# Performance work log

Measured on AMD Instinct MI355X. Metric: run time of the kernel, lower is better.

The kernel has to match this reference:

```python
import jax, jax.numpy as jnp
import numpy as np

E = 1024      # embed_dim
H = 16        # num_heads
HD = E // H   # head_dim = 64
R = 8         # dora rank
T, B = 2048, 2


def setup_inputs() -> dict:
    key = jax.random.key(0)
    ks = jax.random.split(key, 16)
    query = jax.random.normal(ks[0], (T, B, E), dtype=jnp.float32)
    kk = jax.random.normal(ks[1], (T, B, E), dtype=jnp.float32)
    vv = jax.random.normal(ks[2], (T, B, E), dtype=jnp.float32)

    def make_dora(k1, k2, k3, k4):
        w = jax.random.normal(k1, (E, E), dtype=jnp.float32) * (E ** -0.5)
        m = jnp.linalg.norm(w)            # magnitude scalar (Frobenius norm)
        V = w / m                          # frozen direction, ||V||_F = 1
        A = jax.random.normal(k2, (R, E), dtype=jnp.float32) * (E ** -0.5)
        Bm = jax.random.normal(k3, (E, R), dtype=jnp.float32) * 0.01
        b = jax.random.normal(k4, (E,), dtype=jnp.float32) * 0.01
        return m, V, A, Bm, b

    mag_q, dir_q, A_q, B_q, bias_q = make_dora(ks[3], ks[4], ks[5], ks[6])
    mag_v, dir_v, A_v, B_v, bias_v = make_dora(ks[7], ks[8], ks[9], ks[10])
    k_w = jax.random.normal(ks[11], (E, E), dtype=jnp.float32) * (E ** -0.5)
    k_b = jax.random.normal(ks[12], (E,), dtype=jnp.float32) * 0.01
    out_w = jax.random.normal(ks[13], (E, E), dtype=jnp.float32) * (E ** -0.5)
    out_b = jax.random.normal(ks[14], (E,), dtype=jnp.float32) * 0.01
    return dict(query=query, key=kk, value=vv,
                mag_q=mag_q, dir_q=dir_q, A_q=A_q, B_q=B_q, bias_q=bias_q,
                mag_v=mag_v, dir_v=dir_v, A_v=A_v, B_v=B_v, bias_v=bias_v,
                k_w=k_w, k_b=k_b, out_w=out_w, out_b=out_b)


def _dora_linear(x, m, V, A, Bm, b):
    # W_eff = m * (V + B@A) / (||V + B@A||_F + 1e-8); out = x @ W_eff.T + b
    Vu = V + Bm @ A                      # [E, E]
    W = (m / (jnp.linalg.norm(Vu) + 1e-8)) * Vu
    return x @ W.T + b


def reference(query, key, value, mag_q, dir_q, A_q, B_q, bias_q,
              mag_v, dir_v, A_v, B_v, bias_v, k_w, k_b, out_w, out_b):
    # NOTE: source module ignores `key`/`value` and derives k, v from `query`.
    Tq, Bq, _ = query.shape
    q = _dora_linear(query, mag_q, dir_q, A_q, B_q, bias_q)   # [T, B, E]
    k = query @ k_w.T + k_b                                    # frozen K proj
    v = _dora_linear(query, mag_v, dir_v, A_v, B_v, bias_v)
    # (T, B, E) -> (B*H, T, HD), matching torch reshape/transpose
    q = q.reshape(Tq, Bq * H, HD).transpose(1, 0, 2)
    k = k.reshape(Tq, Bq * H, HD).transpose(1, 0, 2)
    v = v.reshape(Tq, Bq * H, HD).transpose(1, 0, 2)
    scale = HD ** -0.5
    attn = jnp.einsum('nqd,nkd->nqk', q, k) * scale            # [B*H, T, T]
    attn = jax.nn.softmax(attn, axis=-1)                       # dropout p=0
    out = jnp.einsum('nqk,nkd->nqd', attn, v)                  # [B*H, T, HD]
    out = out.transpose(1, 0, 2).reshape(Tq, Bq, E)
    out = out @ out_w.T + out_b
    return out
```

## Files before the change

kernel.cpp:

```cpp
#include <hip/hip_runtime.h>
#include <hip/hip_bf16.h>

#define E_DIM 1024
#define T_DIM 2048
#define B_DIM 2
#define H_DIM 16
#define HD_DIM 64
#define R_DIM 8
#define M_ROWS (T_DIM * B_DIM)
#define LOG2E 1.4426950408889634f

typedef __attribute__((ext_vector_type(8))) short bf16x8;
typedef __attribute__((ext_vector_type(4))) short bf16x4;
typedef __attribute__((ext_vector_type(4))) float f32x4;
typedef __attribute__((ext_vector_type(2))) unsigned uint2v;

#if __has_builtin(__builtin_amdgcn_exp2f)
#define EXP2F(x) __builtin_amdgcn_exp2f(x)
#else
#define EXP2F(x) exp2f(x)
#endif

__device__ __forceinline__ unsigned short f2bf(float f) {
  unsigned int u = __builtin_bit_cast(unsigned int, f);
  u += 0x7FFFu + ((u >> 16) & 1u);
  return (unsigned short)(u >> 16);
}

__device__ __forceinline__ unsigned cvt_pk_bf16(float lo, float hi) {
  unsigned r;
  asm("v_cvt_pk_bf16_f32 %0, %1, %2" : "=v"(r) : "v"(lo), "v"(hi));
  return r;
}

__device__ __forceinline__ f32x4 mfma16(bf16x4 a, bf16x4 b, f32x4 c) {
#if __has_builtin(__builtin_amdgcn_mfma_f32_16x16x16bf16_1k)
  return __builtin_amdgcn_mfma_f32_16x16x16bf16_1k(a, b, c, 0, 0, 0);
#elif __has_builtin(__builtin_amdgcn_mfma_f32_16x16x16_bf16)
  return __builtin_amdgcn_mfma_f32_16x16x16_bf16(a, b, c, 0, 0, 0);
#else
  asm("v_mfma_f32_16x16x16_bf16 %0, %1, %2, %0" : "+v"(c) : "v"(a), "v"(b));
  return c;
#endif
}

__device__ __forceinline__ void glds16(const unsigned short* g, unsigned short* l) {
  __builtin_amdgcn_global_load_lds(
      (__attribute__((address_space(1))) void*)(g),
      (__attribute__((address_space(3))) void*)(l), 16, 0, 0);
}

__global__ __launch_bounds__(256) void prep(
    const float* __restrict__ query, const float* __restrict__ k_w,
    const float* __restrict__ out_w,
    const float* __restrict__ dir_q, const float* __restrict__ A_q, const float* __restrict__ B_q,
    const float* __restrict__ dir_v, const float* __restrict__ A_v, const float* __restrict__ B_v,
    unsigned short* __restrict__ qA_bf, unsigned short* __restrict__ kw_bf,
    unsigned short* __restrict__ ow_bf,
    unsigned short* __restrict__ Wq, unsigned short* __restrict__ Wv,
    float* __restrict__ partials) {
  const int bid = blockIdx.x;
  if (bid < 6144) {
    int u = bid * 256 + threadIdx.x;
    const float* src;
    unsigned short* dst;
    if (u < 1048576) { src = query; dst = qA_bf; }
    else if (u < 1310720) { src = k_w; dst = kw_bf; u -= 1048576; }
    else { src = out_w; dst = ow_bf; u -= 1310720; }
    float4 f = reinterpret_cast<const float4*>(src)[u];
    ushort4 o;
    o.x = f2bf(f.x); o.y = f2bf(f.y); o.z = f2bf(f.z); o.w = f2bf(f.w);
    reinterpret_cast<ushort4*>(dst)[u] = o;
    return;
  }
  const int bid2 = bid - 6144;
  const int mat = bid2 >> 8, bx = bid2 & 255;
  const float* __restrict__ dir = mat ? dir_v : dir_q;
  const float* __restrict__ Am  = mat ? A_v   : A_q;
  const float* __restrict__ Bm  = mat ? B_v   : B_q;
  unsigned short* __restrict__ W = mat ? Wv : Wq;

  float sum = 0.0f;
  for (int idx = bx * 256 + threadIdx.x; idx < E_DIM * E_DIM; idx += 256 * 256) {
    int i = idx >> 10;
    int j = idx & (E_DIM - 1);
    float v = dir[idx];
#pragma unroll
    for (int r = 0; r < R_DIM; ++r)
      v += Bm[i * R_DIM + r] * Am[r * E_DIM + j];
    W[idx] = f2bf(v);
    sum += v * v;
  }
#pragma unroll
  for (int off = 32; off > 0; off >>= 1) sum += __shfl_down(sum, off);
  __shared__ float red[4];
  if ((threadIdx.x & 63) == 0) red[threadIdx.x >> 6] = sum;
  __syncthreads();
  if (threadIdx.x == 0)
    partials[mat * 256 + bx] = (red[0] + red[1]) + (red[2] + red[3]);
}

__global__ __launch_bounds__(256) void dora_pass2(
    const float* __restrict__ partials, const float* __restrict__ mag_q,
    const float* __restrict__ mag_v, float* __restrict__ scales) {
  __shared__ float red[4];
  for (int mat = 0; mat < 2; ++mat) {
    float s = partials[mat * 256 + threadIdx.x];
#pragma unroll
    for (int off = 32; off > 0; off >>= 1) s += __shfl_down(s, off);
    if ((threadIdx.x & 63) == 0) red[threadIdx.x >> 6] = s;
    __syncthreads();
    if (threadIdx.x == 0) {
      float tot = (red[0] + red[1]) + (red[2] + red[3]);
      float m = mat ? mag_v[0] : mag_q[0];
      scales[mat] = m / (sqrtf(tot) + 1e-8f);
    }
    __syncthreads();
  }
}

template <int OUT_MODE>
__device__ __forceinline__ void gemm_bt_core(
    const unsigned short* __restrict__ A, const unsigned short* __restrict__ W,
    const float* __restrict__ bias, float scale, float bscale,
    void* __restrict__ Cptr, int bm, int bn) {
  __shared__ unsigned short As[128 * 32];
  __shared__ unsigned short Bs[128 * 32];
  const int tid = threadIdx.x;
  const int w = tid >> 6, lane = tid & 63;
  const int lr = lane & 15, lg = lane >> 4;
  const int wm = w >> 1, wn = w & 1;

  f32x4 acc[4][4];
#pragma unroll
  for (int i = 0; i < 4; ++i)
#pragma unroll
    for (int j = 0; j < 4; ++j) acc[i][j] = (f32x4){0.f, 0.f, 0.f, 0.f};

  const int c0u = tid, c1u = 256 + tid;
  const int r0 = c0u >> 2, o0 = (c0u & 3) * 8;
  const int r1 = c1u >> 2, o1 = (c1u & 3) * 8;

  for (int k0 = 0; k0 < E_DIM; k0 += 32) {
    glds16(A + (size_t)(bm + r0) * E_DIM + k0 + o0, As + c0u * 8);
    glds16(W + (size_t)(bn + r0) * E_DIM + k0 + o0, Bs + c0u * 8);
    glds16(A + (size_t)(bm + r1) * E_DIM + k0 + o1, As + c1u * 8);
    glds16(W + (size_t)(bn + r1) * E_DIM + k0 + o1, Bs + c1u * 8);
    __syncthreads();

    bf16x8 af[4], bf[4];
#pragma unroll
    for (int i = 0; i < 4; ++i)
      af[i] = *reinterpret_cast<const bf16x8*>(As + (wm * 64 + i * 16 + lr) * 32 + lg * 8);
#pragma unroll
    for (int j = 0; j < 4; ++j)
      bf[j] = *reinterpret_cast<const bf16x8*>(Bs + (wn * 64 + j * 16 + lr) * 32 + lg * 8);
#pragma unroll
    for (int i = 0; i < 4; ++i)
#pragma unroll
      for (int j = 0; j < 4; ++j)
        acc[i][j] = __builtin_amdgcn_mfma_f32_16x16x32_bf16(af[i], bf[j], acc[i][j], 0, 0, 0);
    __syncthreads();
  }

  if (OUT_MODE == 2) {
#pragma unroll
    for (int i = 0; i < 4; ++i) {
      int rowbase = bm + wm * 64 + i * 16 + lg * 4;
      float4 bb = *reinterpret_cast<const float4*>(&bias[rowbase]);
      float bbv[4] = {bb.x, bb.y, bb.z, bb.w};
#pragma unroll
      for (int j = 0; j < 4; ++j) {
        int xrow = bn + wn * 64 + j * 16 + lr;
        int t = xrow >> 1, bsel = xrow & 1;
#pragma unroll
        for (int rr = 0; rr < 4; ++rr) {
          int wrow = rowbase + rr;
          float v = scale * acc[i][j][rr] + bbv[rr];
          int nn = (bsel << 4) | (wrow >> 6);
          int d = wrow & 63;
          reinterpret_cast<unsigned short*>(Cptr)[((size_t)nn * HD_DIM + d) * T_DIM + t] = f2bf(v);
        }
      }
    }
  } else {
#pragma unroll
    for (int i = 0; i < 4; ++i) {
      int row = bm + wm * 64 + i * 16 + lg * 4;
#pragma unroll
      for (int j = 0; j < 4; ++j) {
        int col = bn + wn * 64 + j * 16 + lr;
        float bv = bias[col] * bscale;
#pragma unroll
        for (int r = 0; r < 4; ++r) {
          float v = scale * acc[i][j][r] + bv;
          if (OUT_MODE == 1)
            reinterpret_cast<unsigned short*>(Cptr)[(size_t)(row + r) * E_DIM + col] = f2bf(v);
          else
            reinterpret_cast<float*>(Cptr)[(size_t)(row + r) * E_DIM + col] = v;
        }
      }
    }
  }
}

__global__ __launch_bounds__(256) void gemm_qkv(
    const unsigned short* __restrict__ Abf,
    const unsigned short* __restrict__ Wq, const unsigned short* __restrict__ Wk,
    const unsigned short* __restrict__ Wv,
    const float* __restrict__ bias_q, const float* __restrict__ k_b,
    const float* __restrict__ bias_v, const float* __restrict__ scales,
    unsigned short* __restrict__ qbuf, unsigned short* __restrict__ kbuf,
    unsigned short* __restrict__ vT) {
  const int bid = blockIdx.x;
  const int swz = (bid & 7) * 96 + (bid >> 3);
  if (swz < 512) {
    const int mat = swz >> 8;
    const int idx = swz & 255;
    const int bm = (idx >> 3) * 128, bn = (idx & 7) * 128;
    if (mat == 0) {
      const float sm = 0.125f * LOG2E;
      gemm_bt_core<1>(Abf, Wq, bias_q, scales[0] * sm, sm, qbuf, bm, bn);
    } else {
      gemm_bt_core<1>(Abf, Wk, k_b, 1.0f, 1.0f, kbuf, bm, bn);
    }
  } else {
    const int idx = swz - 512;
    gemm_bt_core<2>(Wv, Abf, bias_v, scales[1], 1.0f, vT,
                    (idx >> 5) * 128, (idx & 31) * 128);
  }
}

__global__ __launch_bounds__(256) void gemm_out(
    const unsigned short* __restrict__ Abf, const unsigned short* __restrict__ Wo,
    const float* __restrict__ bias, float* __restrict__ out) {
  const int bid = blockIdx.x;
  const int swz = (bid & 7) * 32 + (bid >> 3);
  gemm_bt_core<0>(Abf, Wo, bias, 1.0f, 1.0f, out, (swz >> 3) * 128, (swz & 7) * 128);
}

#define LDP 72

__global__ __launch_bounds__(512, 2) void attn_mfma(
    const unsigned short* __restrict__ qb, const unsigned short* __restrict__ kb,
    const unsigned short* __restrict__ vT, unsigned short* __restrict__ ob) {
  __shared__ unsigned short Ks[64 * LDP];
  __shared__ unsigned short Vt[64 * LDP];
  const int n = blockIdx.y, b = n >> 4, col0 = (n & 15) * HD_DIM;
  const int tid = threadIdx.x, w = tid >> 6, lane = tid & 63;
  const int lr = lane & 15, lg = lane >> 4;
  const int q0 = blockIdx.x * 256 + w * 32;

  bf16x8 qf[2][2];
#pragma unroll
  for (int rf = 0; rf < 2; ++rf)
#pragma unroll
    for (int ks = 0; ks < 2; ++ks)
      qf[rf][ks] = *reinterpret_cast<const bf16x8*>(
          qb + ((size_t)(q0 + rf * 16 + lr) * B_DIM + b) * E_DIM + col0 + ks * 32 + lg * 8);

  f32x4 accO[2][4];
#pragma unroll
  for (int rf = 0; rf < 2; ++rf)
#pragma unroll
    for (int df = 0; df < 4; ++df) accO[rf][df] = (f32x4){0.f, 0.f, 0.f, 0.f};
  float mrun0 = -1e30f, mrun1 = -1e30f, lrun0 = 0.f, lrun1 = 0.f;

  const int sr = tid >> 3, sc = (tid & 7) * 8;
  float4 rk, rv;
  rk = *reinterpret_cast<const float4*>(kb + ((size_t)sr * B_DIM + b) * E_DIM + col0 + sc);
  rv = *reinterpret_cast<const float4*>(vT + ((size_t)n * HD_DIM + sr) * T_DIM + sc);

  for (int kt = 0; kt < T_DIM; kt += 64) {
    __syncthreads();
    *reinterpret_cast<float4*>(Ks + sr * LDP + sc) = rk;
    *reinterpret_cast<float4*>(Vt + sr * LDP + sc) = rv;
    __syncthreads();
    if (kt + 64 < T_DIM) {
      int kt2 = kt + 64;
      rk = *reinterpret_cast<const float4*>(kb + ((size_t)(kt2 + sr) * B_DIM + b) * E_DIM + col0 + sc);
      rv = *reinterpret_cast<const float4*>(vT + ((size_t)n * HD_DIM + sr) * T_DIM + kt2 + sc);
    }

    f32x4 s[4][2];
#pragma unroll
    for (int kf = 0; kf < 4; ++kf)
#pragma unroll
      for (int rf = 0; rf < 2; ++rf) s[kf][rf] = (f32x4){0.f, 0.f, 0.f, 0.f};
    __builtin_amdgcn_s_setprio(1);
#pragma unroll
    for (int ks = 0; ks < 2; ++ks)
#pragma unroll
      for (int kf = 0; kf < 4; ++kf) {
        bf16x8 kfr = *reinterpret_cast<const bf16x8*>(Ks + (kf * 16 + lr) * LDP + ks * 32 + lg * 8);
#pragma unroll
        for (int rf = 0; rf < 2; ++rf)
          s[kf][rf] = __builtin_amdgcn_mfma_f32_16x16x32_bf16(kfr, qf[rf][ks], s[kf][rf], 0, 0, 0);
      }
    __builtin_amdgcn_s_setprio(0);

    float pm0, pm1;
    {
      float a0 = fmaxf(fmaxf(s[0][0][0], s[0][0][1]), fmaxf(s[0][0][2], s[0][0][3]));
      float a1 = fmaxf(fmaxf(s[1][0][0], s[1][0][1]), fmaxf(s[1][0][2], s[1][0][3]));
      float a2 = fmaxf(fmaxf(s[2][0][0], s[2][0][1]), fmaxf(s[2][0][2], s[2][0][3]));
      float a3 = fmaxf(fmaxf(s[3][0][0], s[3][0][1]), fmaxf(s[3][0][2], s[3][0][3]));
      pm0 = fmaxf(fmaxf(a0, a1), fmaxf(a2, a3));
      float b0 = fmaxf(fmaxf(s[0][1][0], s[0][1][1]), fmaxf(s[0][1][2], s[0][1][3]));
      float b1 = fmaxf(fmaxf(s[1][1][0], s[1][1][1]), fmaxf(s[1][1][2], s[1][1][3]));
      float b2 = fmaxf(fmaxf(s[2][1][0], s[2][1][1]), fmaxf(s[2][1][2], s[2][1][3]));
      float b3 = fmaxf(fmaxf(s[3][1][0], s[3][1][1]), fmaxf(s[3][1][2], s[3][1][3]));
      pm1 = fmaxf(fmaxf(b0, b1), fmaxf(b2, b3));
    }
    pm0 = fmaxf(pm0, __shfl_xor(pm0, 16)); pm0 = fmaxf(pm0, __shfl_xor(pm0, 32));
    pm1 = fmaxf(pm1, __shfl_xor(pm1, 16)); pm1 = fmaxf(pm1, __shfl_xor(pm1, 32));

    const int resc = __any((pm0 > mrun0 + 8.0f) || (pm1 > mrun1 + 8.0f));
    float mn0 = mrun0, mn1 = mrun1;
    if (resc) { mn0 = fmaxf(mn0, pm0); mn1 = fmaxf(mn1, pm1); }

#pragma unroll
    for (int kf = 0; kf < 4; ++kf)
#pragma unroll
      for (int r = 0; r < 4; ++r) {
        s[kf][0][r] = EXP2F(s[kf][0][r] - mn0);
        s[kf][1][r] = EXP2F(s[kf][1][r] - mn1);
      }

    bf16x4 pa4[2][4];
#pragma unroll
    for (int rf = 0; rf < 2; ++rf)
#pragma unroll
      for (int kf = 0; kf < 4; ++kf) {
        uint2v u = (uint2v){cvt_pk_bf16(s[kf][rf][0], s[kf][rf][1]),
                            cvt_pk_bf16(s[kf][rf][2], s[kf][rf][3])};
        pa4[rf][kf] = __builtin_bit_cast(bf16x4, u);
      }

    f32x4 u0 = (s[0][0] + s[1][0]) + (s[2][0] + s[3][0]);
    f32x4 u1 = (s[0][1] + s[1][1]) + (s[2][1] + s[3][1]);
    float ps0 = (u0[0] + u0[1]) + (u0[2] + u0[3]);
    float ps1 = (u1[0] + u1[1]) + (u1[2] + u1[3]);
    ps0 += __shfl_xor(ps0, 16); ps0 += __shfl_xor(ps0, 32);
    ps1 += __shfl_xor(ps1, 16); ps1 += __shfl_xor(ps1, 32);

    if (resc) {
      float al0 = EXP2F(mrun0 - mn0), al1 = EXP2F(mrun1 - mn1);
      mrun0 = mn0; mrun1 = mn1;
      lrun0 = lrun0 * al0 + ps0; lrun1 = lrun1 * al1 + ps1;
#pragma unroll
      for (int r = 0; r < 4; ++r) {
        float a0 = __shfl(al0, (lg << 2) | r);
        float a1 = __shfl(al1, (lg << 2) | r);
#pragma unroll
        for (int df = 0; df < 4; ++df) { accO[0][df][r] *= a0; accO[1][df][r] *= a1; }
      }
    } else {
      lrun0 += ps0; lrun1 += ps1;
    }

    __builtin_amdgcn_s_setprio(1);
#pragma unroll
    for (int kf = 0; kf < 4; ++kf) {
#pragma unroll
      for (int df = 0; df < 4; ++df) {
        bf16x4 vf4 = *reinterpret_cast<const bf16x4*>(
            Vt + (df * 16 + lr) * LDP + kf * 16 + lg * 4);
        accO[0][df] = mfma16(pa4[0][kf], vf4, accO[0][df]);
        accO[1][df] = mfma16(pa4[1][kf], vf4, accO[1][df]);
      }
    }
    __builtin_amdgcn_s_setprio(0);
  }

#pragma unroll
  for (int rf = 0; rf < 2; ++rf)
#pragma unroll
    for (int r = 0; r < 4; ++r) {
      float lv = __shfl(rf ? lrun1 : lrun0, (lg << 2) | r);
      float inv = 1.0f / lv;
      int row = q0 + rf * 16 + lg * 4 + r;
      size_t base = ((size_t)row * B_DIM + b) * E_DIM + col0;
#pragma unroll
      for (int df = 0; df < 4; ++df)
        ob[base + df * 16 + lr] = f2bf(accO[rf][df][r] * inv);
    }
}

extern "C" void kernel_launch(void* const* d_in, const int* in_sizes, int n_in,
                              void* d_out, int out_size, void* d_ws, size_t ws_size,
                              hipStream_t stream) {
  const float* query  = (const float*)d_in[0];
  const float* mag_q  = (const float*)d_in[3];
  const float* dir_q  = (const float*)d_in[4];
  const float* A_q    = (const float*)d_in[5];
  const float* B_q    = (const float*)d_in[6];
  const float* bias_q = (const float*)d_in[7];
  const float* mag_v  = (const float*)d_in[8];
  const float* dir_v  = (const float*)d_in[9];
  const float* A_v    = (const float*)d_in[10];
  const float* B_v    = (const float*)d_in[11];
  const float* bias_v = (const float*)d_in[12];
  const float* k_w    = (const float*)d_in[13];
  const float* k_b    = (const float*)d_in[14];
  const float* out_w  = (const float*)d_in[15];
  const float* out_b  = (const float*)d_in[16];
  float* out = (float*)d_out;

  char* ws = (char*)d_ws;
  float* partials = (float*)ws;
  float* scales   = (float*)(ws + 2048);
  unsigned short* qA_bf = (unsigned short*)(ws + 4096);
  unsigned short* wq_bf = qA_bf + (size_t)M_ROWS * E_DIM;
  unsigned short* wv_bf = wq_bf + (size_t)E_DIM * E_DIM;
  unsigned short* kw_bf = wv_bf + (size_t)E_DIM * E_DIM;
  unsigned short* ow_bf = kw_bf + (size_t)E_DIM * E_DIM;
  unsigned short* qbuf  = ow_bf + (size_t)E_DIM * E_DIM;
  unsigned short* kbuf  = qbuf + (size_t)M_ROWS * E_DIM;
  unsigned short* vTbuf = kbuf + (size_t)M_ROWS * E_DIM;
  unsigned short* abuf  = vTbuf + (size_t)M_ROWS * E_DIM;

  prep<<<6656, 256, 0, stream>>>(query, k_w, out_w,
                                 dir_q, A_q, B_q, dir_v, A_v, B_v,
                                 qA_bf, kw_bf, ow_bf, wq_bf, wv_bf, partials);
  dora_pass2<<<1, 256, 0, stream>>>(partials, mag_q, mag_v, scales);

  gemm_qkv<<<768, 256, 0, stream>>>(qA_bf, wq_bf, kw_bf, wv_bf,
                                    bias_q, k_b, bias_v, scales,
                                    qbuf, kbuf, vTbuf);
  attn_mfma<<<dim3(T_DIM / 256, B_DIM * H_DIM), 512, 0, stream>>>(
      qbuf, kbuf, vTbuf, abuf);
  gemm_out<<<256, 256, 0, stream>>>(abuf, ow_bf, out_b, out);
}
```

Before: 161.1 us.

## Fold DoRA norm reduction into QKV GEMM and double attention KV tile

```diff
diff --git a/kernel.cpp b/kernel.cpp
--- a/kernel.cpp
+++ b/kernel.cpp
@@ -100,25 +100,6 @@
     partials[mat * 256 + bx] = (red[0] + red[1]) + (red[2] + red[3]);
 }
 
-__global__ __launch_bounds__(256) void dora_pass2(
-    const float* __restrict__ partials, const float* __restrict__ mag_q,
-    const float* __restrict__ mag_v, float* __restrict__ scales) {
-  __shared__ float red[4];
-  for (int mat = 0; mat < 2; ++mat) {
-    float s = partials[mat * 256 + threadIdx.x];
-#pragma unroll
-    for (int off = 32; off > 0; off >>= 1) s += __shfl_down(s, off);
-    if ((threadIdx.x & 63) == 0) red[threadIdx.x >> 6] = s;
-    __syncthreads();
-    if (threadIdx.x == 0) {
-      float tot = (red[0] + red[1]) + (red[2] + red[3]);
-      float m = mat ? mag_v[0] : mag_q[0];
-      scales[mat] = m / (sqrtf(tot) + 1e-8f);
-    }
-    __syncthreads();
-  }
-}
-
 template <int OUT_MODE>
 __device__ __forceinline__ void gemm_bt_core(
     const unsigned short* __restrict__ A, const unsigned short* __restrict__ W,
@@ -209,24 +190,47 @@
     const unsigned short* __restrict__ Wq, const unsigned short* __restrict__ Wk,
     const unsigned short* __restrict__ Wv,
     const float* __restrict__ bias_q, const float* __restrict__ k_b,
-    const float* __restrict__ bias_v, const float* __restrict__ scales,
+    const float* __restrict__ bias_v,
+    const float* __restrict__ partials, const float* __restrict__ mag_q,
+    const float* __restrict__ mag_v,
     unsigned short* __restrict__ qbuf, unsigned short* __restrict__ kbuf,
     unsigned short* __restrict__ vT) {
   const int bid = blockIdx.x;
   const int swz = (bid & 7) * 96 + (bid >> 3);
-  if (swz < 512) {
-    const int mat = swz >> 8;
-    const int idx = swz & 255;
-    const int bm = (idx >> 3) * 128, bn = (idx & 7) * 128;
+  const int mat = (swz < 256) ? 0 : (swz < 512) ? 1 : 2;
+
+  float scale = 1.0f, bscale = 1.0f;
+  if (mat != 1) {
+    const int sel = (mat == 0) ? 0 : 1;
+    float s = partials[sel * 256 + threadIdx.x];
+#pragma unroll
+    for (int off = 32; off > 0; off >>= 1) s += __shfl_down(s, off);
+    __shared__ float red[4];
+    if ((threadIdx.x & 63) == 0) red[threadIdx.x >> 6] = s;
+    __syncthreads();
+    float tot = (red[0] + red[1]) + (red[2] + red[3]);
+    float m = (mat == 0) ? mag_q[0] : mag_v[0];
+    float sc = m / (sqrtf(tot) + 1e-8f);
     if (mat == 0) {
       const float sm = 0.125f * LOG2E;
-      gemm_bt_core<1>(Abf, Wq, bias_q, scales[0] * sm, sm, qbuf, bm, bn);
+      scale = sc * sm; bscale = sm;
     } else {
-      gemm_bt_core<1>(Abf, Wk, k_b, 1.0f, 1.0f, kbuf, bm, bn);
-    }
+      scale = sc;
+    }
+    __syncthreads();
+  }
+
+  if (mat == 0) {
+    const int idx = swz;
+    gemm_bt_core<1>(Abf, Wq, bias_q, scale, bscale, qbuf,
+                    (idx >> 3) * 128, (idx & 7) * 128);
+  } else if (mat == 1) {
+    const int idx = swz - 256;
+    gemm_bt_core<1>(Abf, Wk, k_b, 1.0f, 1.0f, kbuf,
+                    (idx >> 3) * 128, (idx & 7) * 128);
   } else {
     const int idx = swz - 512;
-    gemm_bt_core<2>(Wv, Abf, bias_v, scales[1], 1.0f, vT,
+    gemm_bt_core<2>(Wv, Abf, bias_v, scale, 1.0f, vT,
                     (idx >> 5) * 128, (idx & 31) * 128);
   }
 }
@@ -239,13 +243,14 @@
   gemm_bt_core<0>(Abf, Wo, bias, 1.0f, 1.0f, out, (swz >> 3) * 128, (swz & 7) * 128);
 }
 
-#define LDP 72
+#define LDPK 72
+#define LDPV 136
 
 __global__ __launch_bounds__(512, 2) void attn_mfma(
     const unsigned short* __restrict__ qb, const unsigned short* __restrict__ kb,
     const unsigned short* __restrict__ vT, unsigned short* __restrict__ ob) {
-  __shared__ unsigned short Ks[64 * LDP];
-  __shared__ unsigned short Vt[64 * LDP];
+  __shared__ unsigned short Ks2[128 * LDPK];
+  __shared__ unsigned short Vt2[64 * LDPV];
   const int n = blockIdx.y, b = n >> 4, col0 = (n & 15) * HD_DIM;
   const int tid = threadIdx.x, w = tid >> 6, lane = tid & 63;
   const int lr = lane & 15, lg = lane >> 4;
@@ -266,111 +271,126 @@
     for (int df = 0; df < 4; ++df) accO[rf][df] = (f32x4){0.f, 0.f, 0.f, 0.f};
   float mrun0 = -1e30f, mrun1 = -1e30f, lrun0 = 0.f, lrun1 = 0.f;
 
-  const int sr = tid >> 3, sc = (tid & 7) * 8;
-  float4 rk, rv;
-  rk = *reinterpret_cast<const float4*>(kb + ((size_t)sr * B_DIM + b) * E_DIM + col0 + sc);
-  rv = *reinterpret_cast<const float4*>(vT + ((size_t)n * HD_DIM + sr) * T_DIM + sc);
-
-  for (int kt = 0; kt < T_DIM; kt += 64) {
-    __syncthreads();
-    *reinterpret_cast<float4*>(Ks + sr * LDP + sc) = rk;
-    *reinterpret_cast<float4*>(Vt + sr * LDP + sc) = rv;
-    __syncthreads();
-    if (kt + 64 < T_DIM) {
-      int kt2 = kt + 64;
-      rk = *reinterpret_cast<const float4*>(kb + ((size_t)(kt2 + sr) * B_DIM + b) * E_DIM + col0 + sc);
-      rv = *reinterpret_cast<const float4*>(vT + ((size_t)n * HD_DIM + sr) * T_DIM + kt2 + sc);
-    }
-
-    f32x4 s[4][2];
-#pragma unroll
-    for (int kf = 0; kf < 4; ++kf)
-#pragma unroll
-      for (int rf = 0; rf < 2; ++rf) s[kf][rf] = (f32x4){0.f, 0.f, 0.f, 0.f};
-    __builtin_amdgcn_s_setprio(1);
-#pragma unroll
-    for (int ks = 0; ks < 2; ++ks)
+  const int kr0 = tid >> 3, kc0 = (tid & 7) * 8;
+  const int kr1 = 64 + kr0;
+  const int vd0 = tid >> 4, vc0 = (tid & 15) * 8;
+  const int vd1 = 32 + vd0;
+  float4 rk0, rk1, rv0, rv1;
+  rk0 = *reinterpret_cast<const float4*>(kb + ((size_t)kr0 * B_DIM + b) * E_DIM + col0 + kc0);
+  rk1 = *reinterpret_cast<const float4*>(kb + ((size_t)kr1 * B_DIM + b) * E_DIM + col0 + kc0);
+  rv0 = *reinterpret_cast<const float4*>(vT + ((size_t)n * HD_DIM + vd0) * T_DIM + vc0);
+  rv1 = *reinterpret_cast<const float4*>(vT + ((size_t)n * HD_DIM + vd1) * T_DIM + vc0);
+
+  for (int kt = 0; kt < T_DIM; kt += 128) {
+    __syncthreads();
+    *reinterpret_cast<float4*>(Ks2 + kr0 * LDPK + kc0) = rk0;
+    *reinterpret_cast<float4*>(Ks2 + kr1 * LDPK + kc0) = rk1;
+    *reinterpret_cast<float4*>(Vt2 + vd0 * LDPV + vc0) = rv0;
+    *reinterpret_cast<float4*>(Vt2 + vd1 * LDPV + vc0) = rv1;
+    __syncthreads();
+    if (kt + 128 < T_DIM) {
+      int kt2 = kt + 128;
+      rk0 = *reinterpret_cast<const float4*>(kb + ((size_t)(kt2 + kr0) * B_DIM + b) * E_DIM + col0 + kc0);
+      rk1 = *reinterpret_cast<const float4*>(kb + ((size_t)(kt2 + kr1) * B_DIM + b) * E_DIM + col0 + kc0);
+      rv0 = *reinterpret_cast<const float4*>(vT + ((size_t)n * HD_DIM + vd0) * T_DIM + kt2 + vc0);
+      rv1 = *reinterpret_cast<const float4*>(vT + ((size_t)n * HD_DIM + vd1) * T_DIM + kt2 + vc0);
+    }
+
+#pragma unroll
+    for (int h = 0; h < 2; ++h) {
+      const unsigned short* Kh = Ks2 + h * 64 * LDPK;
+      const unsigned short* Vh = Vt2 + h * 64;
+
+      f32x4 s[4][2];
+#pragma unroll
+      for (int kf = 0; kf < 4; ++kf)
+#pragma unroll
+        for (int rf = 0; rf < 2; ++rf) s[kf][rf] = (f32x4){0.f, 0.f, 0.f, 0.f};
+      __builtin_amdgcn_s_setprio(1);
+#pragma unroll
+      for (int ks = 0; ks < 2; ++ks)
+#pragma unroll
+        for (int kf = 0; kf < 4; ++kf) {
+          bf16x8 kfr = *reinterpret_cast<const bf16x8*>(Kh + (kf * 16 + lr) * LDPK + ks * 32 + lg * 8);
+#pragma unroll
+          for (int rf = 0; rf < 2; ++rf)
+            s[kf][rf] = __builtin_amdgcn_mfma_f32_16x16x32_bf16(kfr, qf[rf][ks], s[kf][rf], 0, 0, 0);
+        }
+      __builtin_amdgcn_s_setprio(0);
+
+      float pm0, pm1;
+      {
+        float a0 = fmaxf(fmaxf(s[0][0][0], s[0][0][1]), fmaxf(s[0][0][2], s[0][0][3]));
+        float a1 = fmaxf(fmaxf(s[1][0][0], s[1][0][1]), fmaxf(s[1][0][2], s[1][0][3]));
+        float a2 = fmaxf(fmaxf(s[2][0][0], s[2][0][1]), fmaxf(s[2][0][2], s[2][0][3]));
+        float a3 = fmaxf(fmaxf(s[3][0][0], s[3][0][1]), fmaxf(s[3][0][2], s[3][0][3]));
+        pm0 = fmaxf(fmaxf(a0, a1), fmaxf(a2, a3));
+        float b0 = fmaxf(fmaxf(s[0][1][0], s[0][1][1]), fmaxf(s[0][1][2], s[0][1][3]));
+        float b1 = fmaxf(fmaxf(s[1][1][0], s[1][1][1]), fmaxf(s[1][1][2], s[1][1][3]));
+        float b2 = fmaxf(fmaxf(s[2][1][0], s[2][1][1]), fmaxf(s[2][1][2], s[2][1][3]));
+        float b3 = fmaxf(fmaxf(s[3][1][0], s[3][1][1]), fmaxf(s[3][1][2], s[3][1][3]));
+        pm1 = fmaxf(fmaxf(b0, b1), fmaxf(b2, b3));
+      }
+      pm0 = fmaxf(pm0, __shfl_xor(pm0, 16)); pm0 = fmaxf(pm0, __shfl_xor(pm0, 32));
+      pm1 = fmaxf(pm1, __shfl_xor(pm1, 16)); pm1 = fmaxf(pm1, __shfl_xor(pm1, 32));
+
+      const int resc = __any((pm0 > mrun0 + 8.0f) || (pm1 > mrun1 + 8.0f));
+      float mn0 = mrun0, mn1 = mrun1;
+      if (resc) { mn0 = fmaxf(mn0, pm0); mn1 = fmaxf(mn1, pm1); }
+
+#pragma unroll
+      for (int kf = 0; kf < 4; ++kf)
+#pragma unroll
+        for (int r = 0; r < 4; ++r) {
+          s[kf][0][r] = EXP2F(s[kf][0][r] - mn0);
+          s[kf][1][r] = EXP2F(s[kf][1][r] - mn1);
+        }
+
+      bf16x4 pa4[2][4];
+#pragma unroll
+      for (int rf = 0; rf < 2; ++rf)
+#pragma unroll
+        for (int kf = 0; kf < 4; ++kf) {
+          uint2v u = (uint2v){cvt_pk_bf16(s[kf][rf][0], s[kf][rf][1]),
+                              cvt_pk_bf16(s[kf][rf][2], s[kf][rf][3])};
+          pa4[rf][kf] = __builtin_bit_cast(bf16x4, u);
+        }
+
+      f32x4 u0 = (s[0][0] + s[1][0]) + (s[2][0] + s[3][0]);
+      f32x4 u1 = (s[0][1] + s[1][1]) + (s[2][1] + s[3][1]);
+      float ps0 = (u0[0] + u0[1]) + (u0[2] + u0[3]);
+      float ps1 = (u1[0] + u1[1]) + (u1[2] + u1[3]);
+      ps0 += __shfl_xor(ps0, 16); ps0 += __shfl_xor(ps0, 32);
+      ps1 += __shfl_xor(ps1, 16); ps1 += __shfl_xor(ps1, 32);
+
+      if (resc) {
+        float al0 = EXP2F(mrun0 - mn0), al1 = EXP2F(mrun1 - mn1);
+        mrun0 = mn0; mrun1 = mn1;
+        lrun0 = lrun0 * al0 + ps0; lrun1 = lrun1 * al1 + ps1;
+#pragma unroll
+        for (int r = 0; r < 4; ++r) {
+          float a0 = __shfl(al0, (lg << 2) | r);
+          float a1 = __shfl(al1, (lg << 2) | r);
+#pragma unroll
+          for (int df = 0; df < 4; ++df) { accO[0][df][r] *= a0; accO[1][df][r] *= a1; }
+        }
+      } else {
+        lrun0 += ps0; lrun1 += ps1;
+      }
+
+      __builtin_amdgcn_s_setprio(1);
 #pragma unroll
       for (int kf = 0; kf < 4; ++kf) {
-        bf16x8 kfr = *reinterpret_cast<const bf16x8*>(Ks + (kf * 16 + lr) * LDP + ks * 32 + lg * 8);
-#pragma unroll
-        for (int rf = 0; rf < 2; ++rf)
-          s[kf][rf] = __builtin_amdgcn_mfma_f32_16x16x32_bf16(kfr, qf[rf][ks], s[kf][rf], 0, 0, 0);
+#pragma unroll
+        for (int df = 0; df < 4; ++df) {
+          bf16x4 vf4 = *reinterpret_cast<const bf16x4*>(
+              Vh + (df * 16 + lr) * LDPV + kf * 16 + lg * 4);
+          accO[0][df] = mfma16(pa4[0][kf], vf4, accO[0][df]);
+          accO[1][df] = mfma16(pa4[1][kf], vf4, accO[1][df]);
+        }
       }
-    __builtin_amdgcn_s_setprio(0);
-
-    float pm0, pm1;
-    {
-      float a0 = fmaxf(fmaxf(s[0][0][0], s[0][0][1]), fmaxf(s[0][0][2], s[0][0][3]));
-      float a1 = fmaxf(fmaxf(s[1][0][0], s[1][0][1]), fmaxf(s[1][0][2], s[1][0][3]));
-      float a2 = fmaxf(fmaxf(s[2][0][0], s[2][0][1]), fmaxf(s[2][0][2], s[2][0][3]));
-      float a3 = fmaxf(fmaxf(s[3][0][0], s[3][0][1]), fmaxf(s[3][0][2], s[3][0][3]));
-      pm0 = fmaxf(fmaxf(a0, a1), fmaxf(a2, a3));
-      float b0 = fmaxf(fmaxf(s[0][1][0], s[0][1][1]), fmaxf(s[0][1][2], s[0][1][3]));
-      float b1 = fmaxf(fmaxf(s[1][1][0], s[1][1][1]), fmaxf(s[1][1][2], s[1][1][3]));
-      float b2 = fmaxf(fmaxf(s[2][1][0], s[2][1][1]), fmaxf(s[2][1][2], s[2][1][3]));
-      float b3 = fmaxf(fmaxf(s[3][1][0], s[3][1][1]), fmaxf(s[3][1][2], s[3][1][3]));
-      pm1 = fmaxf(fmaxf(b0, b1), fmaxf(b2, b3));
-    }
-    pm0 = fmaxf(pm0, __shfl_xor(pm0, 16)); pm0 = fmaxf(pm0, __shfl_xor(pm0, 32));
-    pm1 = fmaxf(pm1, __shfl_xor(pm1, 16)); pm1 = fmaxf(pm1, __shfl_xor(pm1, 32));
-
-    const int resc = __any((pm0 > mrun0 + 8.0f) || (pm1 > mrun1 + 8.0f));
-    float mn0 = mrun0, mn1 = mrun1;
-    if (resc) { mn0 = fmaxf(mn0, pm0); mn1 = fmaxf(mn1, pm1); }
-
-#pragma unroll
-    for (int kf = 0; kf < 4; ++kf)
-#pragma unroll
-      for (int r = 0; r < 4; ++r) {
-        s[kf][0][r] = EXP2F(s[kf][0][r] - mn0);
-        s[kf][1][r] = EXP2F(s[kf][1][r] - mn1);
-      }
-
-    bf16x4 pa4[2][4];
-#pragma unroll
-    for (int rf = 0; rf < 2; ++rf)
-#pragma unroll
-      for (int kf = 0; kf < 4; ++kf) {
-        uint2v u = (uint2v){cvt_pk_bf16(s[kf][rf][0], s[kf][rf][1]),
-                            cvt_pk_bf16(s[kf][rf][2], s[kf][rf][3])};
-        pa4[rf][kf] = __builtin_bit_cast(bf16x4, u);
-      }
-
-    f32x4 u0 = (s[0][0] + s[1][0]) + (s[2][0] + s[3][0]);
-    f32x4 u1 = (s[0][1] + s[1][1]) + (s[2][1] + s[3][1]);
-    float ps0 = (u0[0] + u0[1]) + (u0[2] + u0[3]);
-    float ps1 = (u1[0] + u1[1]) + (u1[2] + u1[3]);
-    ps0 += __shfl_xor(ps0, 16); ps0 += __shfl_xor(ps0, 32);
-    ps1 += __shfl_xor(ps1, 16); ps1 += __shfl_xor(ps1, 32);
-
-    if (resc) {
-      float al0 = EXP2F(mrun0 - mn0), al1 = EXP2F(mrun1 - mn1);
-      mrun0 = mn0; mrun1 = mn1;
-      lrun0 = lrun0 * al0 + ps0; lrun1 = lrun1 * al1 + ps1;
-#pragma unroll
-      for (int r = 0; r < 4; ++r) {
-        float a0 = __shfl(al0, (lg << 2) | r);
-        float a1 = __shfl(al1, (lg << 2) | r);
-#pragma unroll
-        for (int df = 0; df < 4; ++df) { accO[0][df][r] *= a0; accO[1][df][r] *= a1; }
-      }
-    } else {
-      lrun0 += ps0; lrun1 += ps1;
-    }
-
-    __builtin_amdgcn_s_setprio(1);
-#pragma unroll
-    for (int kf = 0; kf < 4; ++kf) {
-#pragma unroll
-      for (int df = 0; df < 4; ++df) {
-        bf16x4 vf4 = *reinterpret_cast<const bf16x4*>(
-            Vt + (df * 16 + lr) * LDP + kf * 16 + lg * 4);
-        accO[0][df] = mfma16(pa4[0][kf], vf4, accO[0][df]);
-        accO[1][df] = mfma16(pa4[1][kf], vf4, accO[1][df]);
-      }
-    }
-    __builtin_amdgcn_s_setprio(0);
+      __builtin_amdgcn_s_setprio(0);
+    }
   }
 
 #pragma unroll
@@ -409,7 +429,6 @@
 
   char* ws = (char*)d_ws;
   float* partials = (float*)ws;
-  float* scales   = (float*)(ws + 2048);
   unsigned short* qA_bf = (unsigned short*)(ws + 4096);
   unsigned short* wq_bf = qA_bf + (size_t)M_ROWS * E_DIM;
   unsigned short* wv_bf = wq_bf + (size_t)E_DIM * E_DIM;
@@ -423,10 +442,10 @@
   prep<<<6656, 256, 0, stream>>>(query, k_w, out_w,
                                  dir_q, A_q, B_q, dir_v, A_v, B_v,
                                  qA_bf, kw_bf, ow_bf, wq_bf, wv_bf, partials);
-  dora_pass2<<<1, 256, 0, stream>>>(partials, mag_q, mag_v, scales);
 
   gemm_qkv<<<768, 256, 0, stream>>>(qA_bf, wq_bf, kw_bf, wv_bf,
-                                    bias_q, k_b, bias_v, scales,
+                                    bias_q, k_b, bias_v,
+                                    partials, mag_q, mag_v,
                                     qbuf, kbuf, vTbuf);
   attn_mfma<<<dim3(T_DIM / 256, B_DIM * H_DIM), 512, 0, stream>>>(
       qbuf, kbuf, vTbuf, abuf);
```

New measurement: 154.6 us. -4.1%, faster.
